# Kernel tuning notes

Hardware: AMD Instinct MI355X
Metric: run time of the kernel (lower is better)

The kernel has to match this reference:

```python
import jax, jax.numpy as jnp
import numpy as np
import math

STEPS = 2  # phase_quant_version='v2'
PI = math.pi


def _masked_abs_mean(x, mask):
    # mean of |x| over mask; 0 if mask empty; clamped to 1e-6 (matches torch code)
    cnt = jnp.sum(mask)
    s = jnp.sum(jnp.abs(x) * mask) / jnp.maximum(cnt, 1).astype(x.dtype)
    s = jnp.where(cnt > 0, s, jnp.zeros((), x.dtype))
    return jnp.maximum(s, jnp.asarray(1e-6, x.dtype))


def _phase_quant_base(w_real, w_imag, temp):
    # temp > 0 path (soft assignment); the hard/STE path is unused for temp>0
    phase = jnp.arctan2(w_imag, w_real)
    real_pos = (phase >= -PI / 4) & (phase < PI / 4)
    real_neg = (phase >= 3 * PI / 4) | (phase < -3 * PI / 4)
    imag_pos = (phase >= PI / 4) & (phase < 3 * PI / 4)
    imag_neg = (phase >= -3 * PI / 4) & (phase < -PI / 4)
    mask_real = real_pos | real_neg
    mask_imag = imag_pos | imag_neg
    s_re = _masked_abs_mean(w_real, mask_real)
    s_im = _masked_abs_mean(w_imag, mask_imag)
    centers = jnp.asarray([0.0, PI / 2, PI, -PI / 2], dtype=phase.dtype)
    d = phase[..., None] - centers  # [N, M, 4]
    delta = jnp.arctan2(jnp.sin(d), jnp.cos(d))
    logits = -(delta * delta)
    prob = jax.nn.softmax(logits / (temp + 1e-6), axis=-1)
    qw_real = (prob[..., 0] - prob[..., 2]) * s_re
    qw_imag = (prob[..., 1] - prob[..., 3]) * s_im
    return qw_real.astype(w_real.dtype), qw_imag.astype(w_imag.dtype)


def _phase_quant_residual(w_real, w_imag, temp, steps):
    qw_real = jnp.zeros_like(w_real)
    qw_imag = jnp.zeros_like(w_imag)
    err_real, err_imag = w_real, w_imag
    for _ in range(steps):
        q_real, q_imag = _phase_quant_base(err_real, err_imag, temp)
        qw_real = qw_real + q_real
        qw_imag = qw_imag + q_imag
        err_real = err_real - q_real
        err_imag = err_imag - q_imag
    return qw_real, qw_imag


def setup_inputs() -> dict:
    key = jax.random.key(0)
    k1, k2 = jax.random.split(key)
    N, M = 4096, 8192
    return {
        "w_real": jax.random.normal(k1, (N, M), dtype=jnp.float32),
        "w_imag": jax.random.normal(k2, (N, M), dtype=jnp.float32),
        "temp": jnp.ones((), dtype=jnp.float32),
    }


def reference(w_real, w_imag, temp):
    return _phase_quant_residual(w_real, w_imag, temp, STEPS)
```

## Files before the change

### kernel.cpp

```cpp
#include <hip/hip_runtime.h>
#include <math.h>


#define NM_PI     3.14159265358979323846f
#define NM_PI2_4  2.46740110027233965468f
#define NM_PISQ   9.86960440108935861883f

#define NBLK 4096

__device__ __forceinline__ float atan_poly(float r) {
  float r2 = r * r;
  float p = fmaf(-0.0851330f, r2, 0.1801410f);
  p = fmaf(p, r2, -0.3302995f);
  p = fmaf(0.0208351f, r2 * r2, p);
  float q = 0.0208351f;
  q = fmaf(q, r2, -0.0851330f);
  q = fmaf(q, r2, 0.1801410f);
  q = fmaf(q, r2, -0.3302995f);
  q = fmaf(q, r2, 0.9998660f);
  (void)p;
  return r * q;
}

__device__ __forceinline__ void soft_dirs(float x, float y, float k_t,
                                          float c1, float c2,
                                          float& dre, float& dim) {
  float ax = fabsf(x), ay = fabsf(y);
  float hi = fmaxf(ax, ay), lo = fminf(ax, ay);
  float r = lo * __builtin_amdgcn_rcpf(fmaxf(hi, 1e-30f));
  float u = atan_poly(r);
  float P = __expf(k_t * u);
  float Pi = __builtin_amdgcn_rcpf(P);
  float wo = c2 * P * P;
  float wp = c1 * P;
  float wq = c1 * Pi;
  float inv_sum = __builtin_amdgcn_rcpf(1.0f + wo + wp + wq);
  float dmaj = (1.0f - wo) * inv_sum;
  float dmin = (wp - wq) * inv_sum;
  bool xdom = (ax >= ay);
  float sx = copysignf(1.0f, x), sy = copysignf(1.0f, y);
  dre = sx * (xdom ? dmaj : dmin);
  dim = sy * (xdom ? dmin : dmaj);
}

__device__ __forceinline__ float finalize_s(float sum, unsigned cnt) {
  float c = (float)(cnt > 0u ? cnt : 1u);
  float s = sum * __builtin_amdgcn_rcpf(c);
  s = (cnt > 0u) ? s : 0.0f;
  return fmaxf(s, 1e-6f);
}

__device__ __forceinline__ void block_reduce3(float& sre, float& sim,
                                              unsigned& cnt) {
  #pragma unroll
  for (int o = 32; o > 0; o >>= 1) {
    sre += __shfl_down(sre, o);
    sim += __shfl_down(sim, o);
    cnt += __shfl_down(cnt, o);
  }
  __shared__ float rf0[16];
  __shared__ float rf1[16];
  __shared__ unsigned ru[16];
  int wave = threadIdx.x >> 6;
  int lane = threadIdx.x & 63;
  int nw = blockDim.x >> 6;
  if (lane == 0) { rf0[wave] = sre; rf1[wave] = sim; ru[wave] = cnt; }
  __syncthreads();
  if (threadIdx.x == 0) {
    float a = rf0[0], b = rf1[0];
    unsigned c = ru[0];
    for (int w = 1; w < nw; ++w) { a += rf0[w]; b += rf1[w]; c += ru[w]; }
    sre = a; sim = b; cnt = c;
  }
}

__global__ __launch_bounds__(256) void pq_k1(const float4* __restrict__ wr,
                                             const float4* __restrict__ wi,
                                             int n4, float* __restrict__ psre,
                                             float* __restrict__ psim,
                                             unsigned* __restrict__ pcnt) {
  float sre = 0.f, sim = 0.f;
  unsigned cnt = 0u;
  int stride = gridDim.x * blockDim.x;
  for (int i = blockIdx.x * blockDim.x + threadIdx.x; i < n4; i += stride) {
    float4 r = wr[i], g = wi[i];
    float xs[4] = {r.x, r.y, r.z, r.w};
    float ys[4] = {g.x, g.y, g.z, g.w};
    #pragma unroll
    for (int k = 0; k < 4; ++k) {
      float ax = fabsf(xs[k]), ay = fabsf(ys[k]);
      bool is_re = (ay <= ax);
      sre += is_re ? ax : 0.f;
      sim += is_re ? 0.f : ay;
      cnt += is_re ? 1u : 0u;
    }
  }
  block_reduce3(sre, sim, cnt);
  if (threadIdx.x == 0) {
    psre[blockIdx.x] = sre;
    psim[blockIdx.x] = sim;
    pcnt[blockIdx.x] = cnt;
  }
}

__global__ __launch_bounds__(1024) void pq_reduce(const float* __restrict__ psre,
                                                  const float* __restrict__ psim,
                                                  const unsigned* __restrict__ pcnt,
                                                  unsigned nm,
                                                  float* __restrict__ finals) {
  float sre = 0.f, sim = 0.f;
  unsigned cnt = 0u;
  for (int i = threadIdx.x; i < NBLK; i += 1024) {
    sre += psre[i];
    sim += psim[i];
    cnt += pcnt[i];
  }
  block_reduce3(sre, sim, cnt);
  if (threadIdx.x == 0) {
    finals[0] = finalize_s(sre, cnt);
    finals[1] = finalize_s(sim, nm - cnt);
  }
}

__global__ __launch_bounds__(256) void pq_k2(const float4* __restrict__ wr,
                                             const float4* __restrict__ wi,
                                             int n4,
                                             const float* __restrict__ temp,
                                             const float* __restrict__ finals1,
                                             float* __restrict__ psre,
                                             float* __restrict__ psim,
                                             unsigned* __restrict__ pcnt) {
  float s_re = finals1[0], s_im = finals1[1];
  float it = __builtin_amdgcn_rcpf(temp[0] + 1e-6f);
  float k_t = NM_PI * it;
  float c1 = __expf(-NM_PI2_4 * it);
  float c2 = __expf(-NM_PISQ * it);
  float sre = 0.f, sim = 0.f;
  unsigned cnt = 0u;
  int stride = gridDim.x * blockDim.x;
  for (int i = blockIdx.x * blockDim.x + threadIdx.x; i < n4; i += stride) {
    float4 r = wr[i], g = wi[i];
    float xs[4] = {r.x, r.y, r.z, r.w};
    float ys[4] = {g.x, g.y, g.z, g.w};
    #pragma unroll
    for (int k = 0; k < 4; ++k) {
      float x = xs[k], y = ys[k];
      float dre, dim;
      soft_dirs(x, y, k_t, c1, c2, dre, dim);
      float er = x - dre * s_re;
      float ei = y - dim * s_im;
      float ax = fabsf(er), ay = fabsf(ei);
      bool is_re = (ay <= ax);
      sre += is_re ? ax : 0.f;
      sim += is_re ? 0.f : ay;
      cnt += is_re ? 1u : 0u;
    }
  }
  block_reduce3(sre, sim, cnt);
  if (threadIdx.x == 0) {
    psre[blockIdx.x] = sre;
    psim[blockIdx.x] = sim;
    pcnt[blockIdx.x] = cnt;
  }
}

__global__ __launch_bounds__(256) void pq_k3(const float4* __restrict__ wr,
                                             const float4* __restrict__ wi,
                                             int n4,
                                             const float* __restrict__ temp,
                                             const float* __restrict__ finals1,
                                             const float* __restrict__ finals2,
                                             float4* __restrict__ out) {
  float s_re1 = finals1[0], s_im1 = finals1[1];
  float s_re2 = finals2[0], s_im2 = finals2[1];
  float it = __builtin_amdgcn_rcpf(temp[0] + 1e-6f);
  float k_t = NM_PI * it;
  float c1 = __expf(-NM_PI2_4 * it);
  float c2 = __expf(-NM_PISQ * it);
  int stride = gridDim.x * blockDim.x;
  for (int i = blockIdx.x * blockDim.x + threadIdx.x; i < n4; i += stride) {
    float4 r = wr[i], g = wi[i];
    float xs[4] = {r.x, r.y, r.z, r.w};
    float ys[4] = {g.x, g.y, g.z, g.w};
    float qr[4], qi[4];
    #pragma unroll
    for (int k = 0; k < 4; ++k) {
      float x = xs[k], y = ys[k];
      float d1re, d1im;
      soft_dirs(x, y, k_t, c1, c2, d1re, d1im);
      float q1r = d1re * s_re1;
      float q1i = d1im * s_im1;
      float er = x - q1r;
      float ei = y - q1i;
      float d2re, d2im;
      soft_dirs(er, ei, k_t, c1, c2, d2re, d2im);
      qr[k] = fmaf(d2re, s_re2, q1r);
      qi[k] = fmaf(d2im, s_im2, q1i);
    }
    float4 o0 = {qr[0], qr[1], qr[2], qr[3]};
    float4 o1 = {qi[0], qi[1], qi[2], qi[3]};
    out[i] = o0;
    out[n4 + i] = o1;
  }
}

extern "C" void kernel_launch(void* const* d_in, const int* in_sizes, int n_in,
                              void* d_out, int out_size, void* d_ws, size_t ws_size,
                              hipStream_t stream) {
  const float4* wr = (const float4*)d_in[0];
  const float4* wi = (const float4*)d_in[1];
  const float* temp = (const float*)d_in[2];
  int nm = in_sizes[0];
  int n4 = nm / 4;

  float* w32 = (float*)d_ws;
  unsigned* u32 = (unsigned*)d_ws;
  float* finals1 = w32 + 0;
  float* finals2 = w32 + 2;
  float* p1_sre = w32 + 8;
  float* p1_sim = p1_sre + NBLK;
  unsigned* p1_cnt = u32 + 8 + 2 * NBLK;
  float* p2_sre = w32 + 8 + 3 * NBLK;
  float* p2_sim = p2_sre + NBLK;
  unsigned* p2_cnt = u32 + 8 + 5 * NBLK;

  dim3 block(256);
  dim3 grid(NBLK);
  pq_k1<<<grid, block, 0, stream>>>(wr, wi, n4, p1_sre, p1_sim, p1_cnt);
  pq_reduce<<<1, 1024, 0, stream>>>(p1_sre, p1_sim, p1_cnt, (unsigned)nm, finals1);
  pq_k2<<<grid, block, 0, stream>>>(wr, wi, n4, temp, finals1,
                                    p2_sre, p2_sim, p2_cnt);
  pq_reduce<<<1, 1024, 0, stream>>>(p2_sre, p2_sim, p2_cnt, (unsigned)nm, finals2);
  pq_k3<<<grid, block, 0, stream>>>(wr, wi, n4, temp, finals1, finals2,
                                    (float4*)d_out);
}
```

Before: 215.8 us.

## Fold partial-sum reductions into consumer kernels and reverse k2 traversal order

Removes the two single-block pq_reduce launches. Every block of pq_k2 and pq_k3 now re-reduces the 4096 per-block partials redundantly to get the scale factors. This trades two serialized tiny launches for extra small reads in every block. pq_k2 also walks its grid-stride loop in reverse, so the data pq_k1 touched last is read first while it may still be in cache.

```diff
diff --git a/kernel.cpp b/kernel.cpp
--- a/kernel.cpp
+++ b/kernel.cpp
@@ -7,18 +7,15 @@
 #define NM_PISQ   9.86960440108935861883f
 
 #define NBLK 4096
+#define TPB  256
 
 __device__ __forceinline__ float atan_poly(float r) {
   float r2 = r * r;
-  float p = fmaf(-0.0851330f, r2, 0.1801410f);
-  p = fmaf(p, r2, -0.3302995f);
-  p = fmaf(0.0208351f, r2 * r2, p);
   float q = 0.0208351f;
   q = fmaf(q, r2, -0.0851330f);
   q = fmaf(q, r2, 0.1801410f);
   q = fmaf(q, r2, -0.3302995f);
   q = fmaf(q, r2, 0.9998660f);
-  (void)p;
   return r * q;
 }
 
@@ -50,31 +47,45 @@
   return fmaxf(s, 1e-6f);
 }
 
-__device__ __forceinline__ void block_reduce3(float& sre, float& sim,
-                                              unsigned& cnt) {
+__device__ __forceinline__ void block_allreduce3(float& sre, float& sim,
+                                                 unsigned& cnt) {
   #pragma unroll
   for (int o = 32; o > 0; o >>= 1) {
     sre += __shfl_down(sre, o);
     sim += __shfl_down(sim, o);
     cnt += __shfl_down(cnt, o);
   }
-  __shared__ float rf0[16];
-  __shared__ float rf1[16];
-  __shared__ unsigned ru[16];
+  __shared__ float rf0[4];
+  __shared__ float rf1[4];
+  __shared__ unsigned ru[4];
   int wave = threadIdx.x >> 6;
   int lane = threadIdx.x & 63;
-  int nw = blockDim.x >> 6;
   if (lane == 0) { rf0[wave] = sre; rf1[wave] = sim; ru[wave] = cnt; }
   __syncthreads();
-  if (threadIdx.x == 0) {
-    float a = rf0[0], b = rf1[0];
-    unsigned c = ru[0];
-    for (int w = 1; w < nw; ++w) { a += rf0[w]; b += rf1[w]; c += ru[w]; }
-    sre = a; sim = b; cnt = c;
-  }
-}
-
-__global__ __launch_bounds__(256) void pq_k1(const float4* __restrict__ wr,
+  sre = rf0[0] + rf0[1] + rf0[2] + rf0[3];
+  sim = rf1[0] + rf1[1] + rf1[2] + rf1[3];
+  cnt = ru[0] + ru[1] + ru[2] + ru[3];
+  __syncthreads();
+}
+
+__device__ __forceinline__ void reduce_partials(const float* __restrict__ psre,
+                                                const float* __restrict__ psim,
+                                                const unsigned* __restrict__ pcnt,
+                                                unsigned nm,
+                                                float& s_re, float& s_im) {
+  float a = 0.f, b = 0.f;
+  unsigned c = 0u;
+  for (int i = threadIdx.x; i < NBLK; i += TPB) {
+    a += psre[i];
+    b += psim[i];
+    c += pcnt[i];
+  }
+  block_allreduce3(a, b, c);
+  s_re = finalize_s(a, c);
+  s_im = finalize_s(b, nm - c);
+}
+
+__global__ __launch_bounds__(TPB) void pq_k1(const float4* __restrict__ wr,
                                              const float4* __restrict__ wi,
                                              int n4, float* __restrict__ psre,
                                              float* __restrict__ psim,
@@ -95,7 +106,7 @@
       cnt += is_re ? 1u : 0u;
     }
   }
-  block_reduce3(sre, sim, cnt);
+  block_allreduce3(sre, sim, cnt);
   if (threadIdx.x == 0) {
     psre[blockIdx.x] = sre;
     psim[blockIdx.x] = sim;
@@ -103,34 +114,20 @@
   }
 }
 
-__global__ __launch_bounds__(1024) void pq_reduce(const float* __restrict__ psre,
-                                                  const float* __restrict__ psim,
-                                                  const unsigned* __restrict__ pcnt,
-                                                  unsigned nm,
-                                                  float* __restrict__ finals) {
-  float sre = 0.f, sim = 0.f;
-  unsigned cnt = 0u;
-  for (int i = threadIdx.x; i < NBLK; i += 1024) {
-    sre += psre[i];
-    sim += psim[i];
-    cnt += pcnt[i];
-  }
-  block_reduce3(sre, sim, cnt);
-  if (threadIdx.x == 0) {
-    finals[0] = finalize_s(sre, cnt);
-    finals[1] = finalize_s(sim, nm - cnt);
-  }
-}
-
-__global__ __launch_bounds__(256) void pq_k2(const float4* __restrict__ wr,
+__global__ __launch_bounds__(TPB) void pq_k2(const float4* __restrict__ wr,
                                              const float4* __restrict__ wi,
                                              int n4,
                                              const float* __restrict__ temp,
-                                             const float* __restrict__ finals1,
+                                             const float* __restrict__ p1sre,
+                                             const float* __restrict__ p1sim,
+                                             const unsigned* __restrict__ p1cnt,
+                                             unsigned nm,
                                              float* __restrict__ psre,
                                              float* __restrict__ psim,
                                              unsigned* __restrict__ pcnt) {
-  float s_re = finals1[0], s_im = finals1[1];
+  float s_re1, s_im1;
+  reduce_partials(p1sre, p1sim, p1cnt, nm, s_re1, s_im1);
+
   float it = __builtin_amdgcn_rcpf(temp[0] + 1e-6f);
   float k_t = NM_PI * it;
   float c1 = __expf(-NM_PI2_4 * it);
@@ -138,25 +135,30 @@
   float sre = 0.f, sim = 0.f;
   unsigned cnt = 0u;
   int stride = gridDim.x * blockDim.x;
-  for (int i = blockIdx.x * blockDim.x + threadIdx.x; i < n4; i += stride) {
-    float4 r = wr[i], g = wi[i];
-    float xs[4] = {r.x, r.y, r.z, r.w};
-    float ys[4] = {g.x, g.y, g.z, g.w};
-    #pragma unroll
-    for (int k = 0; k < 4; ++k) {
-      float x = xs[k], y = ys[k];
-      float dre, dim;
-      soft_dirs(x, y, k_t, c1, c2, dre, dim);
-      float er = x - dre * s_re;
-      float ei = y - dim * s_im;
-      float ax = fabsf(er), ay = fabsf(ei);
-      bool is_re = (ay <= ax);
-      sre += is_re ? ax : 0.f;
-      sim += is_re ? 0.f : ay;
-      cnt += is_re ? 1u : 0u;
+  int tid0 = blockIdx.x * blockDim.x + threadIdx.x;
+  int last_base = ((n4 - 1) / stride) * stride;
+  for (int base = last_base; base >= 0; base -= stride) {
+    int i = tid0 + base;
+    if (i < n4) {
+      float4 r = wr[i], g = wi[i];
+      float xs[4] = {r.x, r.y, r.z, r.w};
+      float ys[4] = {g.x, g.y, g.z, g.w};
+      #pragma unroll
+      for (int k = 0; k < 4; ++k) {
+        float x = xs[k], y = ys[k];
+        float dre, dim;
+        soft_dirs(x, y, k_t, c1, c2, dre, dim);
+        float er = x - dre * s_re1;
+        float ei = y - dim * s_im1;
+        float ax = fabsf(er), ay = fabsf(ei);
+        bool is_re = (ay <= ax);
+        sre += is_re ? ax : 0.f;
+        sim += is_re ? 0.f : ay;
+        cnt += is_re ? 1u : 0u;
+      }
     }
   }
-  block_reduce3(sre, sim, cnt);
+  block_allreduce3(sre, sim, cnt);
   if (threadIdx.x == 0) {
     psre[blockIdx.x] = sre;
     psim[blockIdx.x] = sim;
@@ -164,15 +166,22 @@
   }
 }
 
-__global__ __launch_bounds__(256) void pq_k3(const float4* __restrict__ wr,
+__global__ __launch_bounds__(TPB) void pq_k3(const float4* __restrict__ wr,
                                              const float4* __restrict__ wi,
                                              int n4,
                                              const float* __restrict__ temp,
-                                             const float* __restrict__ finals1,
-                                             const float* __restrict__ finals2,
+                                             const float* __restrict__ p1sre,
+                                             const float* __restrict__ p1sim,
+                                             const unsigned* __restrict__ p1cnt,
+                                             const float* __restrict__ p2sre,
+                                             const float* __restrict__ p2sim,
+                                             const unsigned* __restrict__ p2cnt,
+                                             unsigned nm,
                                              float4* __restrict__ out) {
-  float s_re1 = finals1[0], s_im1 = finals1[1];
-  float s_re2 = finals2[0], s_im2 = finals2[1];
+  float s_re1, s_im1, s_re2, s_im2;
+  reduce_partials(p1sre, p1sim, p1cnt, nm, s_re1, s_im1);
+  reduce_partials(p2sre, p2sim, p2cnt, nm, s_re2, s_im2);
+
   float it = __builtin_amdgcn_rcpf(temp[0] + 1e-6f);
   float k_t = NM_PI * it;
   float c1 = __expf(-NM_PI2_4 * it);
@@ -215,8 +224,6 @@
 
   float* w32 = (float*)d_ws;
   unsigned* u32 = (unsigned*)d_ws;
-  float* finals1 = w32 + 0;
-  float* finals2 = w32 + 2;
   float* p1_sre = w32 + 8;
   float* p1_sim = p1_sre + NBLK;
   unsigned* p1_cnt = u32 + 8 + 2 * NBLK;
@@ -224,13 +231,14 @@
   float* p2_sim = p2_sre + NBLK;
   unsigned* p2_cnt = u32 + 8 + 5 * NBLK;
 
-  dim3 block(256);
+  dim3 block(TPB);
   dim3 grid(NBLK);
   pq_k1<<<grid, block, 0, stream>>>(wr, wi, n4, p1_sre, p1_sim, p1_cnt);
-  pq_reduce<<<1, 1024, 0, stream>>>(p1_sre, p1_sim, p1_cnt, (unsigned)nm, finals1);
-  pq_k2<<<grid, block, 0, stream>>>(wr, wi, n4, temp, finals1,
+  pq_k2<<<grid, block, 0, stream>>>(wr, wi, n4, temp,
+                                    p1_sre, p1_sim, p1_cnt, (unsigned)nm,
                                     p2_sre, p2_sim, p2_cnt);
-  pq_reduce<<<1, 1024, 0, stream>>>(p2_sre, p2_sim, p2_cnt, (unsigned)nm, finals2);
-  pq_k3<<<grid, block, 0, stream>>>(wr, wi, n4, temp, finals1, finals2,
+  pq_k3<<<grid, block, 0, stream>>>(wr, wi, n4, temp,
+                                    p1_sre, p1_sim, p1_cnt,
+                                    p2_sre, p2_sim, p2_cnt, (unsigned)nm,
                                     (float4*)d_out);
 }
```

New measurement: 234.9 us. 1.09x slower.
